# Performance work log

Hardware: AMD Instinct MI355X
Metric: run time of the kernel (lower is better)

The kernel has to match this reference:

```python
import jax, jax.numpy as jnp
import numpy as np

N, K, DIM = 65536, 32, 64


def setup_inputs() -> dict:
    key = jax.random.key(0)
    k1, k2, k3, k4 = jax.random.split(key, 4)
    x = jax.random.normal(k1, (N, DIM), jnp.float32)
    log_pi = jax.random.normal(k2, (K, 1), jnp.float32)
    mu = jax.random.normal(k3, (K, DIM), jnp.float32)
    log_sigma_ = jax.random.normal(k4, (K, DIM, DIM), jnp.float32) / 100.0
    return {"x": x, "log_pi": log_pi, "mu": mu, "log_sigma_": log_sigma_}


def reference(x, log_pi, mu, log_sigma_):
    k, d = mu.shape
    # Faithful to torch: softmax over the size-1 last axis of (K,1) -> all ones.
    pi = jax.nn.softmax(log_pi, axis=-1)  # (K, 1)
    # scale_tril construction: strict lower triangle kept, diagonal -> exp(diag) + 1e-3
    diag = jnp.exp(jnp.diagonal(log_sigma_, axis1=-2, axis2=-1)) + 1e-3  # (K, d)
    L = jnp.tril(log_sigma_, -1) + jnp.eye(d, dtype=x.dtype) * diag[:, None, :]  # (K, d, d)
    # batched MVN log_prob via triangular solve
    diff = x[:, None, :] - mu[None, :, :]            # (N, K, d)
    b = jnp.transpose(diff, (1, 2, 0))               # (K, d, N)
    z = jax.scipy.linalg.solve_triangular(L, b, lower=True)  # (K, d, N)
    maha = jnp.sum(z * z, axis=1)                    # (K, N)
    logdet = jnp.sum(jnp.log(diag), axis=-1)         # (K,)
    logp = -0.5 * (maha + d * jnp.log(2.0 * jnp.pi)) - logdet[:, None]  # (K, N)
    p = jnp.exp(logp).T                              # (N, K)
    return jnp.log(jnp.matmul(p, pi).squeeze())      # (N,)
```

## Files before the change

### kernel.cpp

```cpp
#include <hip/hip_runtime.h>

#define KK 32
#define DD 64
#define NB 65536
#define PAD 68
#define FRAGS 12
#define SLOT (FRAGS * 64)
#define MREF 103.0f

typedef __attribute__((ext_vector_type(8))) short bf16x8;
typedef __attribute__((ext_vector_type(4))) float f32x4;

__device__ inline short f2bf(float f) {
  uint32_t u = __builtin_bit_cast(uint32_t, f);
  uint32_t r = (u + 0x7fffu + ((u >> 16) & 1u)) >> 16;
  return (short)(r & 0xffffu);
}
__device__ inline float bf2f(short h) {
  uint32_t u = ((uint32_t)(unsigned short)h) << 16;
  return __builtin_bit_cast(float, u);
}
__device__ inline uint4 pack8(const short* v) {
  uint4 u;
  u.x = (uint32_t)(unsigned short)v[0] | ((uint32_t)(unsigned short)v[1] << 16);
  u.y = (uint32_t)(unsigned short)v[2] | ((uint32_t)(unsigned short)v[3] << 16);
  u.z = (uint32_t)(unsigned short)v[4] | ((uint32_t)(unsigned short)v[5] << 16);
  u.w = (uint32_t)(unsigned short)v[6] | ((uint32_t)(unsigned short)v[7] << 16);
  return u;
}

__global__ __launch_bounds__(64) void md_prep(const float* __restrict__ ls,
                                              const float* __restrict__ mu,
                                              uint4* __restrict__ Bp,
                                              float* __restrict__ Cc,
                                              float* __restrict__ Kc) {
  __shared__ float Ls[DD * DD];
  __shared__ float Ys[DD * PAD];
  const int k = blockIdx.x, j = threadIdx.x;
  const float* __restrict__ lsk = ls + (size_t)k * DD * DD;

#pragma unroll
  for (int it = 0; it < 16; ++it) {
    const int off = it * 256 + j * 4;
    *(float4*)&Ls[off] = *(const float4*)&lsk[off];
  }
  __syncthreads();

  const float dj = expf(Ls[j * DD + j]) + 1e-3f;
  const float invdj = 1.0f / dj;
  {
    float l = logf(dj);
#pragma unroll
    for (int off = 32; off > 0; off >>= 1) l += __shfl_down(l, off, 64);
    if (j == 0) Kc[k] = fmaf(-0.5f, 64.0f * 1.83787706640934534f, -l);
  }

  float z[DD];
#pragma unroll
  for (int i = 0; i < DD; ++i) {
    float s0 = 0.f, s1 = 0.f, s2 = 0.f, s3 = 0.f;
    int m = 0;
#pragma unroll
    for (; m + 4 <= i; m += 4) {
      const float4 lv = *(const float4*)&Ls[i * DD + m];
      s0 = fmaf(lv.x, z[m + 0], s0);
      s1 = fmaf(lv.y, z[m + 1], s1);
      s2 = fmaf(lv.z, z[m + 2], s2);
      s3 = fmaf(lv.w, z[m + 3], s3);
    }
#pragma unroll
    for (; m < i; ++m) s0 = fmaf(Ls[i * DD + m], z[m], s0);
    const float s = (s0 + s1) + (s2 + s3);
    const float di = __shfl(invdj, i, 64);
    z[i] = (i == j) ? invdj : -s * di;
  }

#pragma unroll
  for (int i = 0; i < DD; ++i) Ys[i * PAD + j] = z[i];
  __syncthreads();

  {
    const float* __restrict__ mk = mu + k * DD;
    float c0 = 0.f, c1 = 0.f, c2 = 0.f, c3 = 0.f;
#pragma unroll
    for (int m = 0; m < DD; m += 4) {
      c0 = fmaf(Ys[j * PAD + m + 0], mk[m + 0], c0);
      c1 = fmaf(Ys[j * PAD + m + 1], mk[m + 1], c1);
      c2 = fmaf(Ys[j * PAD + m + 2], mk[m + 2], c2);
      c3 = fmaf(Ys[j * PAD + m + 3], mk[m + 3], c3);
    }
    Cc[k * DD + j] = (c0 + c1) + (c2 + c3);
  }

  const int col = j & 15, q = j >> 4;
  uint4* slot = Bp + (size_t)k * SLOT;
#pragma unroll
  for (int s = 0; s < 2; ++s) {
#pragma unroll
    for (int ct = 0; ct < 4; ++ct) {
      if (s == 1 && ct < 2) continue;
      const int i = col + 16 * ct;
      const float4 v0 = *(const float4*)&Ys[i * PAD + s * 32 + q * 8];
      const float4 v1 = *(const float4*)&Ys[i * PAD + s * 32 + q * 8 + 4];
      const float f[8] = {v0.x, v0.y, v0.z, v0.w, v1.x, v1.y, v1.z, v1.w};
      short hh[8], ll[8];
#pragma unroll
      for (int jj = 0; jj < 8; ++jj) {
        const short h = f2bf(f[jj]);
        hh[jj] = h;
        ll[jj] = f2bf(f[jj] - bf2f(h));
      }
      const int fi = 2 * ct + (s ? 4 : 0);
      slot[(fi + 0) * 64 + j] = pack8(hh);
      slot[(fi + 1) * 64 + j] = pack8(ll);
    }
  }
}

__global__ __launch_bounds__(256, 2) void md_main(const float* __restrict__ x,
                                                  const uint4* __restrict__ Bp,
                                                  const float* __restrict__ Cc,
                                                  const float* __restrict__ Kc,
                                                  float* __restrict__ P) {
  __shared__ uint4 lds4[2 * SLOT];
  const int tid = threadIdx.x, lane = tid & 63, w = tid >> 6;
  const int quarter = blockIdx.x & 3;
  const int sblk = blockIdx.x >> 2;
  const int base = sblk * 256 + w * 64;
  const int k0 = quarter * 8, k1 = k0 + 8;
  const int col = lane & 15, q = lane >> 4;

  bf16x8 Xh[4][2], Xl[4][2];
#pragma unroll
  for (int Bt = 0; Bt < 4; ++Bt) {
#pragma unroll
    for (int s = 0; s < 2; ++s) {
      const float* src = x + (size_t)(base + Bt * 16 + col) * DD + s * 32 + q * 8;
      const float4 v0 = *(const float4*)src;
      const float4 v1 = *(const float4*)(src + 4);
      const float f[8] = {v0.x, v0.y, v0.z, v0.w, v1.x, v1.y, v1.z, v1.w};
      bf16x8 h, l;
#pragma unroll
      for (int jj = 0; jj < 8; ++jj) {
        const short hb = f2bf(f[jj]);
        h[jj] = hb;
        l[jj] = f2bf(f[jj] - bf2f(hb));
      }
      Xh[Bt][s] = h;
      Xl[Bt][s] = l;
    }
  }

  {
    const uint4* src = Bp + (size_t)k0 * SLOT;
#pragma unroll
    for (int it = 0; it < 3; ++it) lds4[it * 256 + tid] = src[it * 256 + tid];
  }
  __syncthreads();

  float run_s[4] = {0.f, 0.f, 0.f, 0.f};

  int p = 0;
  for (int k = k0; k < k1; ++k) {
    const int kn = (k + 1 < k1) ? k + 1 : k;
    const uint4* gsrc = Bp + (size_t)kn * SLOT;
    const uint4 g0 = gsrc[0 * 256 + tid];
    const uint4 g1 = gsrc[1 * 256 + tid];
    const uint4 g2 = gsrc[2 * 256 + tid];
    const float kc = Kc[k];

    const uint4* buf = &lds4[p * SLOT];
    f32x4 mah[4];
#pragma unroll
    for (int Bt = 0; Bt < 4; ++Bt) mah[Bt] = (f32x4){0.f, 0.f, 0.f, 0.f};

#pragma unroll
    for (int ct = 0; ct < 4; ++ct) {
      const bf16x8 A0h = *(const bf16x8*)&buf[(2 * ct + 0) * 64 + lane];
      const bf16x8 A0l = *(const bf16x8*)&buf[(2 * ct + 1) * 64 + lane];
      bf16x8 A1h{}, A1l{};
      if (ct >= 2) {
        A1h = *(const bf16x8*)&buf[(2 * ct + 4) * 64 + lane];
        A1l = *(const bf16x8*)&buf[(2 * ct + 5) * 64 + lane];
      }
      const f32x4 ci = -*(const f32x4*)&Cc[k * DD + ct * 16 + q * 4];
#pragma unroll
      for (int Bt = 0; Bt < 4; ++Bt) {
        f32x4 z = ci;
        z = __builtin_amdgcn_mfma_f32_16x16x32_bf16(A0h, Xh[Bt][0], z, 0, 0, 0);
        z = __builtin_amdgcn_mfma_f32_16x16x32_bf16(A0l, Xh[Bt][0], z, 0, 0, 0);
        z = __builtin_amdgcn_mfma_f32_16x16x32_bf16(A0h, Xl[Bt][0], z, 0, 0, 0);
        if (ct >= 2) {
          z = __builtin_amdgcn_mfma_f32_16x16x32_bf16(A1h, Xh[Bt][1], z, 0, 0, 0);
          z = __builtin_amdgcn_mfma_f32_16x16x32_bf16(A1l, Xh[Bt][1], z, 0, 0, 0);
          z = __builtin_amdgcn_mfma_f32_16x16x32_bf16(A1h, Xl[Bt][1], z, 0, 0, 0);
        }
        mah[Bt] += z * z;
      }
    }

#pragma unroll
    for (int Bt = 0; Bt < 4; ++Bt) {
      float s = (mah[Bt][0] + mah[Bt][1]) + (mah[Bt][2] + mah[Bt][3]);
      s += __shfl_xor(s, 16, 64);
      s += __shfl_xor(s, 32, 64);
      const float t = fmaf(-0.5f, s, kc);
      run_s[Bt] += __expf(t + MREF);
    }

    if (k + 1 < k1) {
      uint4* dst = &lds4[(1 - p) * SLOT];
      dst[0 * 256 + tid] = g0;
      dst[1 * 256 + tid] = g1;
      dst[2 * 256 + tid] = g2;
      __syncthreads();
      p ^= 1;
    }
  }

  if (q == 0) {
#pragma unroll
    for (int Bt = 0; Bt < 4; ++Bt) {
      const int sid = base + Bt * 16 + col;
      P[quarter * NB + sid] = run_s[Bt];
    }
  }
}

__global__ __launch_bounds__(256) void md_comb(const float* __restrict__ P,
                                               float* __restrict__ out) {
  const int n = blockIdx.x * 256 + threadIdx.x;
  const float S = (P[n] + P[NB + n]) + (P[2 * NB + n] + P[3 * NB + n]);
  out[n] = logf(S) - MREF;
}

extern "C" void kernel_launch(void* const* d_in, const int* in_sizes, int n_in,
                              void* d_out, int out_size, void* d_ws, size_t ws_size,
                              hipStream_t stream) {
  const float* x  = (const float*)d_in[0];
  const float* mu = (const float*)d_in[2];
  const float* ls = (const float*)d_in[3];
  float* out = (float*)d_out;

  char* ws = (char*)d_ws;
  uint4* Bp = (uint4*)ws;
  float* Cc = (float*)(ws + (size_t)KK * SLOT * 16);
  float* Kc = Cc + KK * DD;
  float* P  = Kc + KK;

  md_prep<<<KK, DD, 0, stream>>>(ls, mu, Bp, Cc, Kc);
  md_main<<<1024, 256, 0, stream>>>(x, Bp, Cc, Kc, P);
  md_comb<<<NB / 256, 256, 0, stream>>>(P, out);
}
```

Measured before the change: 119.7 us.

## Load per-component factor fragments directly into registers, drop LDS double buffer

The main kernel no longer stages each component's bf16 factor fragments through a shared-memory double buffer with block-wide barriers. Each lane now loads its 12 fragments straight from global memory into a register double buffer, prefetching the next component while computing the current one, with the component loop fully unrolled. This removes LDS traffic and per-component __syncthreads. In exchange every wave issues its own redundant global (mostly L2/L1-hit) loads and register pressure rises by 24 uint4 values, which may hurt occupancy under launch_bounds(256,2).

```diff
diff --git a/kernel.cpp b/kernel.cpp
--- a/kernel.cpp
+++ b/kernel.cpp
@@ -122,12 +122,11 @@
                                                   const float* __restrict__ Cc,
                                                   const float* __restrict__ Kc,
                                                   float* __restrict__ P) {
-  __shared__ uint4 lds4[2 * SLOT];
   const int tid = threadIdx.x, lane = tid & 63, w = tid >> 6;
   const int quarter = blockIdx.x & 3;
   const int sblk = blockIdx.x >> 2;
   const int base = sblk * 256 + w * 64;
-  const int k0 = quarter * 8, k1 = k0 + 8;
+  const int k0 = quarter * 8;
   const int col = lane & 15, q = lane >> 4;
 
   bf16x8 Xh[4][2], Xl[4][2];
@@ -151,37 +150,38 @@
     }
   }
 
-  {
-    const uint4* src = Bp + (size_t)k0 * SLOT;
-#pragma unroll
-    for (int it = 0; it < 3; ++it) lds4[it * 256 + tid] = src[it * 256 + tid];
-  }
-  __syncthreads();
+  const uint4* __restrict__ Bl = Bp + (size_t)k0 * SLOT + lane;
+
+  uint4 F0[FRAGS], F1[FRAGS];
+#pragma unroll
+  for (int fi = 0; fi < FRAGS; ++fi) F0[fi] = Bl[fi * 64];
 
   float run_s[4] = {0.f, 0.f, 0.f, 0.f};
 
-  int p = 0;
-  for (int k = k0; k < k1; ++k) {
-    const int kn = (k + 1 < k1) ? k + 1 : k;
-    const uint4* gsrc = Bp + (size_t)kn * SLOT;
-    const uint4 g0 = gsrc[0 * 256 + tid];
-    const uint4 g1 = gsrc[1 * 256 + tid];
-    const uint4 g2 = gsrc[2 * 256 + tid];
+#pragma unroll
+  for (int kk = 0; kk < 8; ++kk) {
+    const int k = k0 + kk;
+    const uint4* cur = (kk & 1) ? F1 : F0;
+    uint4* nxt = (kk & 1) ? F0 : F1;
+    if (kk < 7) {
+      const uint4* __restrict__ src = Bl + (size_t)(kk + 1) * SLOT;
+#pragma unroll
+      for (int fi = 0; fi < FRAGS; ++fi) nxt[fi] = src[fi * 64];
+    }
     const float kc = Kc[k];
 
-    const uint4* buf = &lds4[p * SLOT];
     f32x4 mah[4];
 #pragma unroll
     for (int Bt = 0; Bt < 4; ++Bt) mah[Bt] = (f32x4){0.f, 0.f, 0.f, 0.f};
 
 #pragma unroll
     for (int ct = 0; ct < 4; ++ct) {
-      const bf16x8 A0h = *(const bf16x8*)&buf[(2 * ct + 0) * 64 + lane];
-      const bf16x8 A0l = *(const bf16x8*)&buf[(2 * ct + 1) * 64 + lane];
+      const bf16x8 A0h = __builtin_bit_cast(bf16x8, cur[2 * ct + 0]);
+      const bf16x8 A0l = __builtin_bit_cast(bf16x8, cur[2 * ct + 1]);
       bf16x8 A1h{}, A1l{};
       if (ct >= 2) {
-        A1h = *(const bf16x8*)&buf[(2 * ct + 4) * 64 + lane];
-        A1l = *(const bf16x8*)&buf[(2 * ct + 5) * 64 + lane];
+        A1h = __builtin_bit_cast(bf16x8, cur[2 * ct + 4]);
+        A1l = __builtin_bit_cast(bf16x8, cur[2 * ct + 5]);
       }
       const f32x4 ci = -*(const f32x4*)&Cc[k * DD + ct * 16 + q * 4];
 #pragma unroll
@@ -207,15 +207,6 @@
       const float t = fmaf(-0.5f, s, kc);
       run_s[Bt] += __expf(t + MREF);
     }
-
-    if (k + 1 < k1) {
-      uint4* dst = &lds4[(1 - p) * SLOT];
-      dst[0 * 256 + tid] = g0;
-      dst[1 * 256 + tid] = g1;
-      dst[2 * 256 + tid] = g2;
-      __syncthreads();
-      p ^= 1;
-    }
   }
 
   if (q == 0) {
```

Result: no change. 121.3 us (+1.3%).
